# Optimization experiments

Measured on AMD Instinct MI355X. Metric: run time of the kernel, lower is better.

## Reference

```python
import jax, jax.numpy as jnp
import numpy as np

N = 500_000      # total observations
D = 40           # per-observation feature dim
S = 2048         # number of segments (time series)
WIDTH = 128      # psi hidden width
LATENT = 128     # latent width
DOT = 64         # dot_prod_dim
HEADS = 4        # n_heads


def setup_inputs() -> dict:
    key = jax.random.key(0)
    ks = jax.random.split(key, 12)

    def he(k, shape):
        fan_in = shape[0]
        lim = np.sqrt(6.0 / fan_in)
        return jax.random.uniform(k, shape, jnp.float32, -lim, lim)

    inputs = jax.random.normal(ks[0], (N, D), jnp.float32)
    segment_ids = jnp.sort(jax.random.randint(ks[1], (N,), 0, S))
    lengths = jax.random.randint(ks[2], (S,), 0, 300)
    return {
        "inputs": inputs,
        "segment_ids": segment_ids,
        "lengths": lengths,
        "W1": he(ks[3], (D, WIDTH)),      "b1": jnp.zeros((WIDTH,), jnp.float32),
        "W2": he(ks[4], (WIDTH, WIDTH)), "b2": jnp.zeros((WIDTH,), jnp.float32),
        "W3": he(ks[5], (WIDTH, LATENT)),"b3": jnp.zeros((LATENT,), jnp.float32),
        "Wr": he(ks[6], (LATENT, LATENT)),"br": jnp.zeros((LATENT,), jnp.float32),
        "W_k": he(ks[7], (LATENT + D, DOT * HEADS)),
        "W_q": jax.random.normal(ks[8], (HEADS, DOT), jnp.float32) * 0.02,
    }


def segment_softmax(x, seg, num_segments):
    # x: [N, H]; softmax over elements sharing the same segment id
    m = jax.ops.segment_max(x, seg, num_segments, indices_are_sorted=True)
    e = jnp.exp(x - m[seg])
    denom = jax.ops.segment_sum(e, seg, num_segments, indices_are_sorted=True)
    return e / denom[seg]


def reference(inputs, segment_ids, lengths, W1, b1, W2, b2, W3, b3, Wr, br, W_k, W_q):
    relu = jax.nn.relu
    # psi: 2 hidden dense layers + latent projection (all relu)
    h = relu(inputs @ W1 + b1)
    h = relu(h @ W2 + b2)
    enc = relu(h @ W3 + b3)                                   # [N, LATENT]
    # segment mean aggregation
    sums = jax.ops.segment_sum(enc, segment_ids, S, indices_are_sorted=True)
    counts = jax.ops.segment_sum(jnp.ones((enc.shape[0], 1), enc.dtype),
                                 segment_ids, S, indices_are_sorted=True)
    agg = sums / jnp.maximum(counts, 1.0)                      # [S, LATENT]
    agg = relu(agg @ Wr + br)                                  # rho
    # broadcast back and combine
    combined = jnp.concatenate([inputs, agg[segment_ids]], axis=-1)  # [N, D+LATENT]
    keys = (combined @ W_k).reshape(-1, HEADS, DOT)            # split+stack == reshape
    preattn = jnp.einsum('nhd,hd->nh', keys, W_q) / jnp.sqrt(jnp.float32(DOT))
    attn = segment_softmax(preattn, segment_ids, S)            # [N, H]
    # match original: list of per-head [N, 1] tensors -> stacked [H, N, 1]
    return jnp.transpose(attn)[..., None]
```

## Files before the change

### kernel.cpp

```cpp
#include <hip/hip_runtime.h>
#include <math.h>


#define NROWS 500000
#define DIM 40
#define NSEG 2048
#define DOTD 64
#define NH 4
#define BLOCK 256
#define CACHE_ROWS 2

__global__ __launch_bounds__(BLOCK) void init_kernel(
    const float* __restrict__ Wk,
    const float* __restrict__ Wq,
    int* __restrict__ seg_start,
    int* __restrict__ seg_end,
    float* __restrict__ wxg)
{
    const int tid = (int)(blockIdx.x * blockDim.x + threadIdx.x);
    if (tid < NSEG) { seg_start[tid] = 0; seg_end[tid] = 0; }
    if (tid < DIM * NH) {
        const int d = tid >> 2;
        const int h = tid & 3;
        const float* wkp = Wk + d * (NH * DOTD) + h * DOTD;
        const float* wqp = Wq + h * DOTD;
        float acc = 0.f;
        #pragma unroll
        for (int j = 0; j < DOTD; ++j) acc += wkp[j] * wqp[j];
        wxg[tid] = acc * 0.125f;
    }
}

__global__ __launch_bounds__(BLOCK) void boundary_kernel(
    const int* __restrict__ seg,
    int* __restrict__ seg_start,
    int* __restrict__ seg_end)
{
    const int n = (int)(blockIdx.x * blockDim.x + threadIdx.x);
    if (n >= NROWS) return;
    const int s = seg[n];
    if (n == 0 || seg[n - 1] != s) seg_start[s] = n;
    if (n == NROWS - 1 || seg[n + 1] != s) seg_end[s] = n + 1;
}

__global__ __launch_bounds__(BLOCK) void seg_attn_kernel(
    const float* __restrict__ x,
    const int* __restrict__ seg_start,
    const int* __restrict__ seg_end,
    const float* __restrict__ wxg,
    float* __restrict__ out)
{
    __shared__ float wx[DIM][NH];
    __shared__ float redbuf[BLOCK / 64][NH];
    __shared__ float mshare[NH];
    __shared__ float dshare[NH];

    const int tid = (int)threadIdx.x;
    if (tid < DIM * NH) wx[tid >> 2][tid & 3] = wxg[tid];
    __syncthreads();

    const int s = (int)blockIdx.x;
    const int start = seg_start[s];
    const int end = seg_end[s];
    const int rows = end - start;
    if (rows <= 0) return;

    float cache[CACHE_ROWS][NH];
    float lmax[NH];
    #pragma unroll
    for (int h = 0; h < NH; ++h) lmax[h] = -3.0e38f;

    for (int i = tid, it = 0; i < rows; i += BLOCK, ++it) {
        const float4* xr = (const float4*)(x + (size_t)(start + i) * DIM);
        float acc[NH] = {0.f, 0.f, 0.f, 0.f};
        #pragma unroll
        for (int q = 0; q < DIM / 4; ++q) {
            const float4 v = xr[q];
            #pragma unroll
            for (int h = 0; h < NH; ++h) {
                acc[h] += v.x * wx[4 * q + 0][h];
                acc[h] += v.y * wx[4 * q + 1][h];
                acc[h] += v.z * wx[4 * q + 2][h];
                acc[h] += v.w * wx[4 * q + 3][h];
            }
        }
        #pragma unroll
        for (int h = 0; h < NH; ++h) {
            if (it < CACHE_ROWS) cache[it][h] = acc[h];
            lmax[h] = fmaxf(lmax[h], acc[h]);
        }
    }

    #pragma unroll
    for (int h = 0; h < NH; ++h) {
        float v = lmax[h];
        #pragma unroll
        for (int off = 32; off > 0; off >>= 1) v = fmaxf(v, __shfl_xor(v, off, 64));
        if ((tid & 63) == 0) redbuf[tid >> 6][h] = v;
    }
    __syncthreads();
    if (tid < NH) {
        mshare[tid] = fmaxf(fmaxf(redbuf[0][tid], redbuf[1][tid]),
                            fmaxf(redbuf[2][tid], redbuf[3][tid]));
    }
    __syncthreads();
    float m[NH];
    #pragma unroll
    for (int h = 0; h < NH; ++h) m[h] = mshare[h];

    float lsum[NH] = {0.f, 0.f, 0.f, 0.f};
    for (int i = tid, it = 0; i < rows; i += BLOCK, ++it) {
        float e[NH];
        if (it < CACHE_ROWS) {
            #pragma unroll
            for (int h = 0; h < NH; ++h) {
                e[h] = __expf(cache[it][h] - m[h]);
                cache[it][h] = e[h];
            }
        } else {
            const float4* xr = (const float4*)(x + (size_t)(start + i) * DIM);
            float acc[NH] = {0.f, 0.f, 0.f, 0.f};
            for (int q = 0; q < DIM / 4; ++q) {
                const float4 v = xr[q];
                for (int h = 0; h < NH; ++h) {
                    acc[h] += v.x * wx[4 * q + 0][h] + v.y * wx[4 * q + 1][h]
                            + v.z * wx[4 * q + 2][h] + v.w * wx[4 * q + 3][h];
                }
            }
            for (int h = 0; h < NH; ++h) e[h] = __expf(acc[h] - m[h]);
        }
        #pragma unroll
        for (int h = 0; h < NH; ++h) lsum[h] += e[h];
    }
    __syncthreads();
    #pragma unroll
    for (int h = 0; h < NH; ++h) {
        float v = lsum[h];
        #pragma unroll
        for (int off = 32; off > 0; off >>= 1) v += __shfl_xor(v, off, 64);
        if ((tid & 63) == 0) redbuf[tid >> 6][h] = v;
    }
    __syncthreads();
    if (tid < NH) {
        dshare[tid] = 1.0f / (redbuf[0][tid] + redbuf[1][tid] +
                              redbuf[2][tid] + redbuf[3][tid]);
    }
    __syncthreads();
    float rden[NH];
    #pragma unroll
    for (int h = 0; h < NH; ++h) rden[h] = dshare[h];

    for (int i = tid, it = 0; i < rows; i += BLOCK, ++it) {
        float e[NH];
        if (it < CACHE_ROWS) {
            #pragma unroll
            for (int h = 0; h < NH; ++h) e[h] = cache[it][h];
        } else {
            const float4* xr = (const float4*)(x + (size_t)(start + i) * DIM);
            float acc[NH] = {0.f, 0.f, 0.f, 0.f};
            for (int q = 0; q < DIM / 4; ++q) {
                const float4 v = xr[q];
                for (int h = 0; h < NH; ++h) {
                    acc[h] += v.x * wx[4 * q + 0][h] + v.y * wx[4 * q + 1][h]
                            + v.z * wx[4 * q + 2][h] + v.w * wx[4 * q + 3][h];
                }
            }
            for (int h = 0; h < NH; ++h) e[h] = __expf(acc[h] - m[h]);
        }
        const int n = start + i;
        #pragma unroll
        for (int h = 0; h < NH; ++h) {
            out[(size_t)h * NROWS + n] = e[h] * rden[h];
        }
    }
}

extern "C" void kernel_launch(void* const* d_in, const int* in_sizes, int n_in,
                              void* d_out, int out_size, void* d_ws, size_t ws_size,
                              hipStream_t stream) {
    const float* x  = (const float*)d_in[0];
    const int* seg  = (const int*)d_in[1];
    const float* Wk = (const float*)d_in[11];
    const float* Wq = (const float*)d_in[12];
    float* out = (float*)d_out;

    int* seg_start = (int*)d_ws;
    int* seg_end   = seg_start + NSEG;
    float* wxg     = (float*)(seg_end + NSEG);

    hipLaunchKernelGGL(init_kernel, dim3((NSEG + BLOCK - 1) / BLOCK), dim3(BLOCK),
                       0, stream, Wk, Wq, seg_start, seg_end, wxg);
    hipLaunchKernelGGL(boundary_kernel, dim3((NROWS + BLOCK - 1) / BLOCK), dim3(BLOCK),
                       0, stream, seg, seg_start, seg_end);
    hipLaunchKernelGGL(seg_attn_kernel, dim3(NSEG), dim3(BLOCK), 0, stream,
                       x, seg_start, seg_end, wxg, out);
}
```

Before: 164.1 us.

## Map one wavefront per segment and merge init with boundary detection

The segment-softmax kernel now gives each segment a single 64-lane wavefront, four per block, instead of a whole 256-thread block. This drops the cross-wave shared-memory reductions and block barriers, and each lane caches up to six rows of logits in registers so x is read again less often. The init and boundary kernels are merged into one prep kernel that fills empty segments explicitly instead of zeroing first, removing one launch. Each wavefront now does serial work proportional to its segment length (about 244 rows on average), which lengthens the per-segment critical path and raises register use.

```diff
diff --git a/kernel.cpp b/kernel.cpp
--- a/kernel.cpp
+++ b/kernel.cpp
@@ -8,18 +8,21 @@
 #define DOTD 64
 #define NH 4
 #define BLOCK 256
-#define CACHE_ROWS 2
+#define SEG_PER_BLOCK 4
+#define CACHE_IT 6
 
-__global__ __launch_bounds__(BLOCK) void init_kernel(
+__global__ __launch_bounds__(BLOCK) void prep_kernel(
+    const int* __restrict__ seg,
     const float* __restrict__ Wk,
     const float* __restrict__ Wq,
     int* __restrict__ seg_start,
     int* __restrict__ seg_end,
     float* __restrict__ wxg)
 {
-    const int tid = (int)(blockIdx.x * blockDim.x + threadIdx.x);
-    if (tid < NSEG) { seg_start[tid] = 0; seg_end[tid] = 0; }
-    if (tid < DIM * NH) {
+    const int tid = (int)threadIdx.x;
+    const int n = (int)(blockIdx.x * BLOCK + tid);
+
+    if (blockIdx.x == 0 && tid < DIM * NH) {
         const int d = tid >> 2;
         const int h = tid & 3;
         const float* wkp = Wk + d * (NH * DOTD) + h * DOTD;
@@ -29,18 +32,25 @@
         for (int j = 0; j < DOTD; ++j) acc += wkp[j] * wqp[j];
         wxg[tid] = acc * 0.125f;
     }
-}
 
-__global__ __launch_bounds__(BLOCK) void boundary_kernel(
-    const int* __restrict__ seg,
-    int* __restrict__ seg_start,
-    int* __restrict__ seg_end)
-{
-    const int n = (int)(blockIdx.x * blockDim.x + threadIdx.x);
-    if (n >= NROWS) return;
-    const int s = seg[n];
-    if (n == 0 || seg[n - 1] != s) seg_start[s] = n;
-    if (n == NROWS - 1 || seg[n + 1] != s) seg_end[s] = n + 1;
+    if (n < NROWS) {
+        const int s = seg[n];
+        if (n == 0) {
+            seg_start[s] = 0;
+            for (int t = 0; t < s; ++t) { seg_start[t] = 0; seg_end[t] = 0; }
+        } else {
+            const int sp = seg[n - 1];
+            if (sp != s) {
+                seg_start[s] = n;
+                seg_end[sp] = n;
+                for (int t = sp + 1; t < s; ++t) { seg_start[t] = n; seg_end[t] = n; }
+            }
+        }
+        if (n == NROWS - 1) {
+            seg_end[s] = NROWS;
+            for (int t = s + 1; t < NSEG; ++t) { seg_start[t] = NROWS; seg_end[t] = NROWS; }
+        }
+    }
 }
 
 __global__ __launch_bounds__(BLOCK) void seg_attn_kernel(
@@ -51,126 +61,117 @@
     float* __restrict__ out)
 {
     __shared__ float wx[DIM][NH];
-    __shared__ float redbuf[BLOCK / 64][NH];
-    __shared__ float mshare[NH];
-    __shared__ float dshare[NH];
 
     const int tid = (int)threadIdx.x;
     if (tid < DIM * NH) wx[tid >> 2][tid & 3] = wxg[tid];
     __syncthreads();
 
-    const int s = (int)blockIdx.x;
+    const int lane = tid & 63;
+    const int s = (int)blockIdx.x * SEG_PER_BLOCK + (tid >> 6);
     const int start = seg_start[s];
     const int end = seg_end[s];
     const int rows = end - start;
     if (rows <= 0) return;
+    const int iters = (rows + 63) >> 6;
 
-    float cache[CACHE_ROWS][NH];
+    float cache[CACHE_IT][NH];
     float lmax[NH];
     #pragma unroll
     for (int h = 0; h < NH; ++h) lmax[h] = -3.0e38f;
 
-    for (int i = tid, it = 0; i < rows; i += BLOCK, ++it) {
-        const float4* xr = (const float4*)(x + (size_t)(start + i) * DIM);
-        float acc[NH] = {0.f, 0.f, 0.f, 0.f};
-        #pragma unroll
-        for (int q = 0; q < DIM / 4; ++q) {
-            const float4 v = xr[q];
+    for (int it = 0; it < iters; ++it) {
+        const int i = it * 64 + lane;
+        if (i < rows) {
+            const float4* xr = (const float4*)(x + (size_t)(start + i) * DIM);
+            float acc[NH] = {0.f, 0.f, 0.f, 0.f};
+            #pragma unroll
+            for (int q = 0; q < DIM / 4; ++q) {
+                const float4 v = xr[q];
+                #pragma unroll
+                for (int h = 0; h < NH; ++h) {
+                    acc[h] += v.x * wx[4 * q + 0][h];
+                    acc[h] += v.y * wx[4 * q + 1][h];
+                    acc[h] += v.z * wx[4 * q + 2][h];
+                    acc[h] += v.w * wx[4 * q + 3][h];
+                }
+            }
             #pragma unroll
             for (int h = 0; h < NH; ++h) {
-                acc[h] += v.x * wx[4 * q + 0][h];
-                acc[h] += v.y * wx[4 * q + 1][h];
-                acc[h] += v.z * wx[4 * q + 2][h];
-                acc[h] += v.w * wx[4 * q + 3][h];
+                if (it < CACHE_IT) cache[it][h] = acc[h];
+                lmax[h] = fmaxf(lmax[h], acc[h]);
             }
-        }
-        #pragma unroll
-        for (int h = 0; h < NH; ++h) {
-            if (it < CACHE_ROWS) cache[it][h] = acc[h];
-            lmax[h] = fmaxf(lmax[h], acc[h]);
         }
     }
 
+    float m[NH];
     #pragma unroll
     for (int h = 0; h < NH; ++h) {
         float v = lmax[h];
         #pragma unroll
         for (int off = 32; off > 0; off >>= 1) v = fmaxf(v, __shfl_xor(v, off, 64));
-        if ((tid & 63) == 0) redbuf[tid >> 6][h] = v;
+        m[h] = v;
     }
-    __syncthreads();
-    if (tid < NH) {
-        mshare[tid] = fmaxf(fmaxf(redbuf[0][tid], redbuf[1][tid]),
-                            fmaxf(redbuf[2][tid], redbuf[3][tid]));
-    }
-    __syncthreads();
-    float m[NH];
-    #pragma unroll
-    for (int h = 0; h < NH; ++h) m[h] = mshare[h];
 
     float lsum[NH] = {0.f, 0.f, 0.f, 0.f};
-    for (int i = tid, it = 0; i < rows; i += BLOCK, ++it) {
-        float e[NH];
-        if (it < CACHE_ROWS) {
+    for (int it = 0; it < iters; ++it) {
+        const int i = it * 64 + lane;
+        if (i < rows) {
+            float e[NH];
+            if (it < CACHE_IT) {
+                #pragma unroll
+                for (int h = 0; h < NH; ++h) {
+                    e[h] = __expf(cache[it][h] - m[h]);
+                    cache[it][h] = e[h];
+                }
+            } else {
+                const float4* xr = (const float4*)(x + (size_t)(start + i) * DIM);
+                float acc[NH] = {0.f, 0.f, 0.f, 0.f};
+                for (int q = 0; q < DIM / 4; ++q) {
+                    const float4 v = xr[q];
+                    for (int h = 0; h < NH; ++h) {
+                        acc[h] += v.x * wx[4 * q + 0][h] + v.y * wx[4 * q + 1][h]
+                                + v.z * wx[4 * q + 2][h] + v.w * wx[4 * q + 3][h];
+                    }
+                }
+                for (int h = 0; h < NH; ++h) e[h] = __expf(acc[h] - m[h]);
+            }
             #pragma unroll
-            for (int h = 0; h < NH; ++h) {
-                e[h] = __expf(cache[it][h] - m[h]);
-                cache[it][h] = e[h];
-            }
-        } else {
-            const float4* xr = (const float4*)(x + (size_t)(start + i) * DIM);
-            float acc[NH] = {0.f, 0.f, 0.f, 0.f};
-            for (int q = 0; q < DIM / 4; ++q) {
-                const float4 v = xr[q];
-                for (int h = 0; h < NH; ++h) {
-                    acc[h] += v.x * wx[4 * q + 0][h] + v.y * wx[4 * q + 1][h]
-                            + v.z * wx[4 * q + 2][h] + v.w * wx[4 * q + 3][h];
-                }
-            }
-            for (int h = 0; h < NH; ++h) e[h] = __expf(acc[h] - m[h]);
+            for (int h = 0; h < NH; ++h) lsum[h] += e[h];
         }
-        #pragma unroll
-        for (int h = 0; h < NH; ++h) lsum[h] += e[h];
     }
-    __syncthreads();
+    float rden[NH];
     #pragma unroll
     for (int h = 0; h < NH; ++h) {
         float v = lsum[h];
         #pragma unroll
         for (int off = 32; off > 0; off >>= 1) v += __shfl_xor(v, off, 64);
-        if ((tid & 63) == 0) redbuf[tid >> 6][h] = v;
+        rden[h] = 1.0f / v;
     }
-    __syncthreads();
-    if (tid < NH) {
-        dshare[tid] = 1.0f / (redbuf[0][tid] + redbuf[1][tid] +
-                              redbuf[2][tid] + redbuf[3][tid]);
-    }
-    __syncthreads();
-    float rden[NH];
-    #pragma unroll
-    for (int h = 0; h < NH; ++h) rden[h] = dshare[h];
 
-    for (int i = tid, it = 0; i < rows; i += BLOCK, ++it) {
-        float e[NH];
-        if (it < CACHE_ROWS) {
+    for (int it = 0; it < iters; ++it) {
+        const int i = it * 64 + lane;
+        if (i < rows) {
+            float e[NH];
+            if (it < CACHE_IT) {
+                #pragma unroll
+                for (int h = 0; h < NH; ++h) e[h] = cache[it][h];
+            } else {
+                const float4* xr = (const float4*)(x + (size_t)(start + i) * DIM);
+                float acc[NH] = {0.f, 0.f, 0.f, 0.f};
+                for (int q = 0; q < DIM / 4; ++q) {
+                    const float4 v = xr[q];
+                    for (int h = 0; h < NH; ++h) {
+                        acc[h] += v.x * wx[4 * q + 0][h] + v.y * wx[4 * q + 1][h]
+                                + v.z * wx[4 * q + 2][h] + v.w * wx[4 * q + 3][h];
+                    }
+                }
+                for (int h = 0; h < NH; ++h) e[h] = __expf(acc[h] - m[h]);
+            }
+            const int n = start + i;
             #pragma unroll
-            for (int h = 0; h < NH; ++h) e[h] = cache[it][h];
-        } else {
-            const float4* xr = (const float4*)(x + (size_t)(start + i) * DIM);
-            float acc[NH] = {0.f, 0.f, 0.f, 0.f};
-            for (int q = 0; q < DIM / 4; ++q) {
-                const float4 v = xr[q];
-                for (int h = 0; h < NH; ++h) {
-                    acc[h] += v.x * wx[4 * q + 0][h] + v.y * wx[4 * q + 1][h]
-                            + v.z * wx[4 * q + 2][h] + v.w * wx[4 * q + 3][h];
-                }
+            for (int h = 0; h < NH; ++h) {
+                out[(size_t)h * NROWS + n] = e[h] * rden[h];
             }
-            for (int h = 0; h < NH; ++h) e[h] = __expf(acc[h] - m[h]);
-        }
-        const int n = start + i;
-        #pragma unroll
-        for (int h = 0; h < NH; ++h) {
-            out[(size_t)h * NROWS + n] = e[h] * rden[h];
         }
     }
 }
@@ -188,10 +189,8 @@
     int* seg_end   = seg_start + NSEG;
     float* wxg     = (float*)(seg_end + NSEG);
 
-    hipLaunchKernelGGL(init_kernel, dim3((NSEG + BLOCK - 1) / BLOCK), dim3(BLOCK),
-                       0, stream, Wk, Wq, seg_start, seg_end, wxg);
-    hipLaunchKernelGGL(boundary_kernel, dim3((NROWS + BLOCK - 1) / BLOCK), dim3(BLOCK),
-                       0, stream, seg, seg_start, seg_end);
-    hipLaunchKernelGGL(seg_attn_kernel, dim3(NSEG), dim3(BLOCK), 0, stream,
-                       x, seg_start, seg_end, wxg, out);
+    hipLaunchKernelGGL(prep_kernel, dim3((NROWS + BLOCK - 1) / BLOCK), dim3(BLOCK),
+                       0, stream, seg, Wk, Wq, seg_start, seg_end, wxg);
+    hipLaunchKernelGGL(seg_attn_kernel, dim3(NSEG / SEG_PER_BLOCK), dim3(BLOCK),
+                       0, stream, x, seg_start, seg_end, wxg, out);
 }
```

New measurement: 142.0 us. 1.15x faster.
